# Kernel tuning notes

Measured on AMD Instinct MI355X. Metric: run time of the kernel, lower is better.

Reference implementation:

```python
import jax, jax.numpy as jnp
import numpy as np

WEIGHT = 1.0
EPS = 1e-10


def _high_mask(h, w):
    # Boolean mask: True = high-frequency region (outside center rectangle after fftshift)
    mask = np.ones((h, w), dtype=np.float32)
    ch, cw = h // 2, w // 2
    mask[ch - h // 8: ch + h // 8, cw - w // 8: cw + w // 8] = 0.0
    return jnp.asarray(mask)


def _high_freq_psd(img):
    # img: (B, 3, H, W) in [-1, 1] -> per-image mean log10 PSD over high-freq region, shape (B,)
    gray = 0.299 * img[:, 0] + 0.587 * img[:, 1] + 0.114 * img[:, 2]  # (B, H, W)
    gray = (gray + 1.0) / 2.0
    fft = jnp.fft.fft2(gray)                       # batched complex FFT over last two dims
    fft = jnp.fft.fftshift(fft, axes=(-2, -1))
    psd_log = jnp.log10(jnp.abs(fft) ** 2 + EPS)   # (B, H, W)
    h, w = gray.shape[-2:]
    mask = _high_mask(h, w)
    return jnp.sum(psd_log * mask, axis=(-2, -1)) / jnp.sum(mask)


def setup_inputs() -> dict:
    key = jax.random.key(0)
    k1, k2 = jax.random.split(key)
    B, C, H, W = 32, 3, 512, 512
    generated = jax.random.normal(k1, (B, C, H, W), dtype=jnp.float32)
    target = jax.random.normal(k2, (B, C, H, W), dtype=jnp.float32)
    return {"generated": generated, "target": target}


def reference(generated, target):
    psd_gen = _high_freq_psd(generated)      # (B,)
    psd_target = _high_freq_psd(target)      # (B,)
    loss = jnp.mean(jnp.abs(psd_gen - psd_target))  # F.l1_loss
    return WEIGHT * loss
```

## Files before the change

### kernel.cpp

```cpp
#include <hip/hip_runtime.h>
#include <hip/hip_bf16.h>
#include <hip/hip_fp16.h>
#include <math.h>


__device__ double g_partials[64 * 17 * 4];
__device__ __align__(16) __half2 g_ws[(size_t)64 * 256 * 512];

__device__ __forceinline__ float2 cadd(float2 a, float2 b){ return make_float2(a.x+b.x, a.y+b.y); }
__device__ __forceinline__ float2 csub(float2 a, float2 b){ return make_float2(a.x-b.x, a.y-b.y); }
__device__ __forceinline__ float2 cmul(float2 a, float2 b){
  return make_float2(fmaf(a.x, b.x, -(a.y*b.y)), fmaf(a.x, b.y, a.y*b.x));
}
__device__ __forceinline__ float2 mul_mi(float2 a){ return make_float2(a.y, -a.x); }

__device__ __forceinline__ void fft8(float2 v[8]){
  const float S = 0.70710678118654752440f;
  float2 c0=cadd(v[0],v[4]), c1=cadd(v[1],v[5]), c2=cadd(v[2],v[6]), c3=cadd(v[3],v[7]);
  float2 d0=csub(v[0],v[4]);
  float2 t1=csub(v[1],v[5]);
  float2 d1=make_float2(S*(t1.x+t1.y), S*(t1.y-t1.x));
  float2 d2=mul_mi(csub(v[2],v[6]));
  float2 t3=csub(v[3],v[7]);
  float2 d3=make_float2(S*(t3.y-t3.x), -S*(t3.x+t3.y));
  float2 e0=cadd(c0,c2), e1=cadd(c1,c3), f0=csub(c0,c2), f1=mul_mi(csub(c1,c3));
  float2 g0=cadd(d0,d2), g1=cadd(d1,d3), h0=csub(d0,d2), h1=mul_mi(csub(d1,d3));
  v[0]=cadd(e0,e1); v[4]=csub(e0,e1);
  v[2]=cadd(f0,f1); v[6]=csub(f0,f1);
  v[1]=cadd(g0,g1); v[5]=csub(g0,g1);
  v[3]=cadd(h0,h1); v[7]=csub(h0,h1);
}

__device__ __forceinline__ void twiddle8(float2 v[8], float ang){
  float sn, cs;
  __sincosf(ang, &sn, &cs);
  float2 w = make_float2(cs, sn);
  float2 wp = w;
  v[1] = cmul(v[1], wp);
  #pragma unroll
  for (int m = 2; m < 8; ++m){ wp = cmul(wp, w); v[m] = cmul(v[m], wp); }
}

__device__ __forceinline__ int padi(int i){ return i + (i >> 3); }

__device__ __forceinline__ void lds_fence(){
  asm volatile("s_waitcnt lgkmcnt(0)" ::: "memory");
  __builtin_amdgcn_sched_barrier(0);
}

__device__ __forceinline__ void fft512(float2 v[8], float* re, float* im, int t){
  const float TW = -6.28318530717958647692f;
  fft8(v);
  twiddle8(v, TW * (float)t * (1.0f/512.0f));
  lds_fence();
  #pragma unroll
  for (int m = 0; m < 8; ++m){ int a = padi(m*64 + t); re[a] = v[m].x; im[a] = v[m].y; }
  lds_fence();
  const int q = t >> 3, n = t & 7;
  #pragma unroll
  for (int j = 0; j < 8; ++j){ int a = padi(q*64 + n + 8*j); v[j].x = re[a]; v[j].y = im[a]; }
  fft8(v);
  twiddle8(v, TW * (float)n * (1.0f/64.0f));
  lds_fence();
  #pragma unroll
  for (int m = 0; m < 8; ++m){ int a = padi(q*64 + m*8 + n); re[a] = v[m].x; im[a] = v[m].y; }
  lds_fence();
  #pragma unroll
  for (int j = 0; j < 8; ++j){ int a = padi(q*64 + n*8 + j); v[j].x = re[a]; v[j].y = im[a]; }
  fft8(v);
}

#define GRAY1(r,g,b) ((fmaf(0.299f,(r), fmaf(0.587f,(g), 0.114f*(b))) + 1.0f)*0.5f)

__device__ __forceinline__ void dma_pair(const float* base, float* st, int t){
  #pragma unroll
  for (int ch = 0; ch < 3; ++ch){
    const float* pb = base + ch * 262144 + 4*t;
    float* lb = st + ch*1024;
    #pragma unroll
    for (int seg = 0; seg < 4; ++seg){
      __builtin_amdgcn_global_load_lds(
        (const __attribute__((address_space(1))) void*)(pb + seg*256),
        (__attribute__((address_space(3))) void*)(lb + seg*256),
        16, 0, 0);
    }
  }
}

__global__ __launch_bounds__(128)
void k_rowfft(const float* __restrict__ gen, const float* __restrict__ tgt){
  const int wg   = blockIdx.x;
  const int img  = wg >> 4;
  const int bl   = wg & 15;
  const int wave = threadIdx.x >> 6, t = threadIdx.x & 63;
  const int prB  = bl*16 + wave*8;
  const float* src = (img < 32) ? gen : tgt;
  const float* base0 = src + (size_t)(img & 31) * 786432 + (size_t)prB * 1024;

  __shared__ float stage_all[2][2][3072];
  float* stg0 = stage_all[wave][0];
  float* stg1 = stage_all[wave][1];

  const int off = 8*(t & 7) + (t >> 3);

  dma_pair(base0, stg0, t);
  #pragma unroll
  for (int n = 0; n < 8; ++n){
    float* stc = (n & 1) ? stg1 : stg0;
    float* stn = (n & 1) ? stg0 : stg1;
    lds_fence();
    if (n < 7) dma_pair(base0 + (size_t)(n+1)*1024, stn, t);
    if (n == 0)      { asm volatile("s_waitcnt vmcnt(12)" ::: "memory"); }
    else if (n < 7)  { asm volatile("s_waitcnt vmcnt(20)" ::: "memory"); }
    else             { asm volatile("s_waitcnt vmcnt(8)"  ::: "memory"); }
    __builtin_amdgcn_sched_barrier(0);

    float2 v[8];
    #pragma unroll
    for (int j = 0; j < 8; ++j){
      const int x = t + 64*j;
      v[j] = make_float2(GRAY1(stc[x],     stc[1024+x], stc[2048+x]),
                         GRAY1(stc[512+x], stc[1536+x], stc[2560+x]));
    }
    fft512(v, stc, stc + 1024, t);

    __half2* dst = g_ws + ((size_t)img * 256 + (prB + n)) * 512;
    #pragma unroll
    for (int j = 0; j < 8; ++j) dst[64*j + off] = __floats2half2_rn(v[j].x, v[j].y);
  }
}

__global__ __launch_bounds__(256)
void k_colfft(){
  const int wg   = blockIdx.x;
  const int img  = wg / 17;
  const int blk  = wg - img * 17;
  const int kx0  = blk * 16;
  const int tid  = threadIdx.x;
  const int wave = tid >> 6, t = tid & 63;
  const int ncols = (blk == 16) ? 1 : 16;

  __shared__ __half2 own[16 * 258], mir[16 * 258];
  __shared__ float re_all[4][576], im_all[4][576];
  float* re = re_all[wave];
  float* im = im_all[wave];

  const __half2* zb = g_ws + (size_t)img * 131072;
  #pragma unroll
  for (int it = 0; it < 16; ++it){
    const int idx = it*256 + tid;
    const int p = idx >> 4, e = idx & 15;
    own[e*258 + p] = zb[p*512 + kx0 + e];
    mir[e*258 + p] = zb[p*512 + ((512 - (kx0 + e)) & 511)];
  }
  __syncthreads();

  double acc = 0.0;
  for (int ci = 0; ci < 4; ++ci){
    const int e = wave*4 + ci;
    if (e < ncols){
      const int kx = kx0 + e;
      const bool sub_own = (kx <= 63);
      const bool sub_mir = (kx >= 1) & (kx <= 64);
      const float base = (kx == 0 || kx == 256) ? 1.0f : 2.0f;

      float2 v[8];
      const int u = t >> 1;
      const bool odd = (t & 1);
      #pragma unroll
      for (int j = 0; j < 8; ++j){
        const int p = u + 32*j;
        float2 A = __half22float2(own[e*258 + p]);
        float2 B = __half22float2(mir[e*258 + p]); B.y = -B.y;
        float2 Fe = make_float2((A.x + B.x)*0.5f, (A.y + B.y)*0.5f);
        float2 Fo = mul_mi(make_float2((A.x - B.x)*0.5f, (A.y - B.y)*0.5f));
        v[j] = odd ? Fo : Fe;
      }
      fft512(v, re, im, t);

      #pragma unroll
      for (int j = 0; j < 8; ++j){
        const bool inS  = (j == 0) | (j == 7);
        const bool inSp = (j == 0) | ((j == 1) & (t == 0)) | ((j == 7) & (t != 0));
        float wgt = base;
        if (sub_own & inS)  wgt -= 1.0f;
        if (sub_mir & inSp) wgt -= 1.0f;
        float m2 = fmaf(v[j].x, v[j].x, fmaf(v[j].y, v[j].y, 1e-10f));
        acc += (double)wgt * (double)log10f(m2);
      }
    }
  }
  #pragma unroll
  for (int off = 32; off; off >>= 1) acc += __shfl_down(acc, off);
  if (t == 0) g_partials[((size_t)img * 17 + blk) * 4 + wave] = acc;
}

__global__ __launch_bounds__(256)
void k_finish(float* __restrict__ out){
  const int tid = threadIdx.x;
  const int img = tid >> 2, part = tid & 3;
  const double* p = g_partials + (size_t)img * 68 + part;
  double s = 0.0;
  for (int k = 0; k < 17; ++k) s += p[4*k];
  __shared__ double sm[256];
  sm[tid] = s;
  __syncthreads();
  if ((tid & 3) == 0){
    double tot = sm[tid] + sm[tid+1] + sm[tid+2] + sm[tid+3];
    sm[tid] = tot * (1.0 / 245760.0);
  }
  __syncthreads();
  if (tid < 64){
    double dv = (tid < 32) ? fabs(sm[tid*4] - sm[(tid+32)*4]) : 0.0;
    #pragma unroll
    for (int off = 32; off; off >>= 1) dv += __shfl_down(dv, off);
    if (tid == 0) out[0] = (float)(dv * (1.0 / 32.0));
  }
}

extern "C" void kernel_launch(void* const* d_in, const int* in_sizes, int n_in,
                              void* d_out, int out_size, void* d_ws, size_t ws_size,
                              hipStream_t stream){
  (void)in_sizes; (void)n_in; (void)out_size; (void)d_ws; (void)ws_size;
  const float* gen = (const float*)d_in[0];
  const float* tgt = (const float*)d_in[1];
  float* out = (float*)d_out;

  k_rowfft<<<dim3(64 * 16), dim3(128), 0, stream>>>(gen, tgt);
  k_colfft<<<dim3(64 * 17), dim3(256), 0, stream>>>();
  k_finish<<<dim3(1), dim3(256), 0, stream>>>(out);
}
```

Before: 70.64 us.

## Replace LDS DMA staging with register double-buffered float4 loads in row FFT

The row FFT kernel no longer stages raw RGB rows into LDS through global_load_lds DMA. It loads float4 vectors into two register buffers, converts to gray in registers and writes only the gray values into a small padded LDS area per wave. Blocks grow from 2 to 4 waves and each wave handles 4 row pairs instead of 8. The aim is to cut LDS footprint and traffic and to raise occupancy and parallelism, at the cost of many more VGPRs for the register buffers (96 floats per thread).

```diff
diff --git a/kernel.cpp b/kernel.cpp
--- a/kernel.cpp
+++ b/kernel.cpp
@@ -72,59 +72,68 @@
 
 #define GRAY1(r,g,b) ((fmaf(0.299f,(r), fmaf(0.587f,(g), 0.114f*(b))) + 1.0f)*0.5f)
 
-__device__ __forceinline__ void dma_pair(const float* base, float* st, int t){
-  #pragma unroll
-  for (int ch = 0; ch < 3; ++ch){
-    const float* pb = base + ch * 262144 + 4*t;
-    float* lb = st + ch*1024;
-    #pragma unroll
-    for (int seg = 0; seg < 4; ++seg){
-      __builtin_amdgcn_global_load_lds(
-        (const __attribute__((address_space(1))) void*)(pb + seg*256),
-        (__attribute__((address_space(3))) void*)(lb + seg*256),
-        16, 0, 0);
-    }
-  }
-}
-
-__global__ __launch_bounds__(128)
+__global__ __launch_bounds__(256, 4)
 void k_rowfft(const float* __restrict__ gen, const float* __restrict__ tgt){
   const int wg   = blockIdx.x;
   const int img  = wg >> 4;
   const int bl   = wg & 15;
   const int wave = threadIdx.x >> 6, t = threadIdx.x & 63;
-  const int prB  = bl*16 + wave*8;
+  const int pr0  = bl*16 + wave*4;
   const float* src = (img < 32) ? gen : tgt;
-  const float* base0 = src + (size_t)(img & 31) * 786432 + (size_t)prB * 1024;
-
-  __shared__ float stage_all[2][2][3072];
-  float* stg0 = stage_all[wave][0];
-  float* stg1 = stage_all[wave][1];
+  const float4* f4 = (const float4*)(src + (size_t)(img & 31) * 786432
+                                         + (size_t)pr0 * 1024) + t;
+
+  __shared__ float ex_all[4][1184];
+  float* re = ex_all[wave];
+  float* im = ex_all[wave] + 576;
 
   const int off = 8*(t & 7) + (t >> 3);
 
-  dma_pair(base0, stg0, t);
-  #pragma unroll
-  for (int n = 0; n < 8; ++n){
-    float* stc = (n & 1) ? stg1 : stg0;
-    float* stn = (n & 1) ? stg0 : stg1;
+  float4 bufA[12], bufB[12];
+  #pragma unroll
+  for (int c = 0; c < 3; ++c)
+    #pragma unroll
+    for (int s = 0; s < 4; ++s) bufA[c*4+s] = f4[c*65536 + s*64];
+
+  #pragma unroll
+  for (int n = 0; n < 4; ++n){
+    const float4* cur = (n & 1) ? bufB : bufA;
+    float4*       nxt = (n & 1) ? bufA : bufB;
+
+    #pragma unroll
+    for (int s = 0; s < 2; ++s){
+      const int x = s*256 + 4*t;
+      float4 r = cur[0+s], g = cur[4+s], b = cur[8+s];
+      re[padi(x+0)] = GRAY1(r.x, g.x, b.x);
+      re[padi(x+1)] = GRAY1(r.y, g.y, b.y);
+      re[padi(x+2)] = GRAY1(r.z, g.z, b.z);
+      re[padi(x+3)] = GRAY1(r.w, g.w, b.w);
+      float4 r2 = cur[2+s], g2 = cur[6+s], b2 = cur[10+s];
+      im[padi(x+0)] = GRAY1(r2.x, g2.x, b2.x);
+      im[padi(x+1)] = GRAY1(r2.y, g2.y, b2.y);
+      im[padi(x+2)] = GRAY1(r2.z, g2.z, b2.z);
+      im[padi(x+3)] = GRAY1(r2.w, g2.w, b2.w);
+    }
+
+    if (n < 3){
+      #pragma unroll
+      for (int c = 0; c < 3; ++c)
+        #pragma unroll
+        for (int s = 0; s < 4; ++s)
+          nxt[c*4+s] = f4[(n+1)*256 + c*65536 + s*64];
+      __builtin_amdgcn_sched_barrier(0);
+    }
+
     lds_fence();
-    if (n < 7) dma_pair(base0 + (size_t)(n+1)*1024, stn, t);
-    if (n == 0)      { asm volatile("s_waitcnt vmcnt(12)" ::: "memory"); }
-    else if (n < 7)  { asm volatile("s_waitcnt vmcnt(20)" ::: "memory"); }
-    else             { asm volatile("s_waitcnt vmcnt(8)"  ::: "memory"); }
-    __builtin_amdgcn_sched_barrier(0);
-
     float2 v[8];
     #pragma unroll
     for (int j = 0; j < 8; ++j){
-      const int x = t + 64*j;
-      v[j] = make_float2(GRAY1(stc[x],     stc[1024+x], stc[2048+x]),
-                         GRAY1(stc[512+x], stc[1536+x], stc[2560+x]));
-    }
-    fft512(v, stc, stc + 1024, t);
-
-    __half2* dst = g_ws + ((size_t)img * 256 + (prB + n)) * 512;
+      const int a = padi(t + 64*j);
+      v[j] = make_float2(re[a], im[a]);
+    }
+    fft512(v, re, im, t);
+
+    __half2* dst = g_ws + ((size_t)img * 256 + (pr0 + n)) * 512;
     #pragma unroll
     for (int j = 0; j < 8; ++j) dst[64*j + off] = __floats2half2_rn(v[j].x, v[j].y);
   }
@@ -226,7 +235,7 @@
   const float* tgt = (const float*)d_in[1];
   float* out = (float*)d_out;
 
-  k_rowfft<<<dim3(64 * 16), dim3(128), 0, stream>>>(gen, tgt);
+  k_rowfft<<<dim3(64 * 16), dim3(256), 0, stream>>>(gen, tgt);
   k_colfft<<<dim3(64 * 17), dim3(256), 0, stream>>>();
   k_finish<<<dim3(1), dim3(256), 0, stream>>>(out);
 }
```

Result: slower. 76.43 us (+8.2%).

## Fold final reduction into column FFT via last-block ticket, ping-pong row FFT LDS

Applied to the files above, without the earlier changes.

Removes the separate k_finish launch. The last column-FFT block, found through an atomic ticket counter that the row kernel resets, now performs the final reduction. The row FFT's second LDS transpose writes to a separate staging region, which drops one LDS fence per FFT. This trades a kernel launch and a barrier for an atomic plus threadfences in every column block.

```diff
diff --git a/kernel.cpp b/kernel.cpp
--- a/kernel.cpp
+++ b/kernel.cpp
@@ -5,6 +5,7 @@
 
 
 __device__ double g_partials[64 * 17 * 4];
+__device__ int    g_done;
 __device__ __align__(16) __half2 g_ws[(size_t)64 * 256 * 512];
 
 __device__ __forceinline__ float2 cadd(float2 a, float2 b){ return make_float2(a.x+b.x, a.y+b.y); }
@@ -70,6 +71,28 @@
   fft8(v);
 }
 
+__device__ __forceinline__ void fft512pp(float2 v[8], float* re1, float* im1,
+                                         float* re2, float* im2, int t){
+  const float TW = -6.28318530717958647692f;
+  fft8(v);
+  twiddle8(v, TW * (float)t * (1.0f/512.0f));
+  lds_fence();
+  #pragma unroll
+  for (int m = 0; m < 8; ++m){ int a = padi(m*64 + t); re1[a] = v[m].x; im1[a] = v[m].y; }
+  lds_fence();
+  const int q = t >> 3, n = t & 7;
+  #pragma unroll
+  for (int j = 0; j < 8; ++j){ int a = padi(q*64 + n + 8*j); v[j].x = re1[a]; v[j].y = im1[a]; }
+  fft8(v);
+  twiddle8(v, TW * (float)n * (1.0f/64.0f));
+  #pragma unroll
+  for (int m = 0; m < 8; ++m){ int a = padi(q*64 + m*8 + n); re2[a] = v[m].x; im2[a] = v[m].y; }
+  lds_fence();
+  #pragma unroll
+  for (int j = 0; j < 8; ++j){ int a = padi(q*64 + n*8 + j); v[j].x = re2[a]; v[j].y = im2[a]; }
+  fft8(v);
+}
+
 #define GRAY1(r,g,b) ((fmaf(0.299f,(r), fmaf(0.587f,(g), 0.114f*(b))) + 1.0f)*0.5f)
 
 __device__ __forceinline__ void dma_pair(const float* base, float* st, int t){
@@ -89,6 +112,7 @@
 
 __global__ __launch_bounds__(128)
 void k_rowfft(const float* __restrict__ gen, const float* __restrict__ tgt){
+  if (blockIdx.x == 0 && threadIdx.x == 0) g_done = 0;
   const int wg   = blockIdx.x;
   const int img  = wg >> 4;
   const int bl   = wg & 15;
@@ -122,7 +146,7 @@
       v[j] = make_float2(GRAY1(stc[x],     stc[1024+x], stc[2048+x]),
                          GRAY1(stc[512+x], stc[1536+x], stc[2560+x]));
     }
-    fft512(v, stc, stc + 1024, t);
+    fft512pp(v, stc, stc + 1024, stc + 1600, stc + 2176, t);
 
     __half2* dst = g_ws + ((size_t)img * 256 + (prB + n)) * 512;
     #pragma unroll
@@ -131,7 +155,7 @@
 }
 
 __global__ __launch_bounds__(256)
-void k_colfft(){
+void k_colfft(float* __restrict__ out){
   const int wg   = blockIdx.x;
   const int img  = wg / 17;
   const int blk  = wg - img * 17;
@@ -142,6 +166,7 @@
 
   __shared__ __half2 own[16 * 258], mir[16 * 258];
   __shared__ float re_all[4][576], im_all[4][576];
+  __shared__ int ticket;
   float* re = re_all[wave];
   float* im = im_all[wave];
 
@@ -193,28 +218,31 @@
   #pragma unroll
   for (int off = 32; off; off >>= 1) acc += __shfl_down(acc, off);
   if (t == 0) g_partials[((size_t)img * 17 + blk) * 4 + wave] = acc;
-}
-
-__global__ __launch_bounds__(256)
-void k_finish(float* __restrict__ out){
-  const int tid = threadIdx.x;
-  const int img = tid >> 2, part = tid & 3;
-  const double* p = g_partials + (size_t)img * 68 + part;
-  double s = 0.0;
-  for (int k = 0; k < 17; ++k) s += p[4*k];
-  __shared__ double sm[256];
-  sm[tid] = s;
+
   __syncthreads();
-  if ((tid & 3) == 0){
-    double tot = sm[tid] + sm[tid+1] + sm[tid+2] + sm[tid+3];
-    sm[tid] = tot * (1.0 / 245760.0);
-  }
+  __threadfence();
+  if (tid == 0) ticket = atomicAdd(&g_done, 1);
   __syncthreads();
-  if (tid < 64){
-    double dv = (tid < 32) ? fabs(sm[tid*4] - sm[(tid+32)*4]) : 0.0;
-    #pragma unroll
-    for (int off = 32; off; off >>= 1) dv += __shfl_down(dv, off);
-    if (tid == 0) out[0] = (float)(dv * (1.0 / 32.0));
+  if (ticket == 64*17 - 1){
+    __threadfence();
+    const int fim = tid >> 2, part = tid & 3;
+    const double* p = g_partials + (size_t)fim * 68 + part;
+    double s = 0.0;
+    for (int k = 0; k < 17; ++k) s += p[4*k];
+    __shared__ double sm[256];
+    sm[tid] = s;
+    __syncthreads();
+    if ((tid & 3) == 0){
+      double tot = sm[tid] + sm[tid+1] + sm[tid+2] + sm[tid+3];
+      sm[tid] = tot * (1.0 / 245760.0);
+    }
+    __syncthreads();
+    if (tid < 64){
+      double dv = (tid < 32) ? fabs(sm[tid*4] - sm[(tid+32)*4]) : 0.0;
+      #pragma unroll
+      for (int off = 32; off; off >>= 1) dv += __shfl_down(dv, off);
+      if (tid == 0) out[0] = (float)(dv * (1.0 / 32.0));
+    }
   }
 }
 
@@ -227,6 +255,5 @@
   float* out = (float*)d_out;
 
   k_rowfft<<<dim3(64 * 16), dim3(128), 0, stream>>>(gen, tgt);
-  k_colfft<<<dim3(64 * 17), dim3(256), 0, stream>>>();
-  k_finish<<<dim3(1), dim3(256), 0, stream>>>(out);
-}
+  k_colfft<<<dim3(64 * 17), dim3(256), 0, stream>>>(out);
+}
```

Measured after the change: 133.1 us. 88.4% more time.

## Replace LDS-transposed FFT512 stages with cross-lane shuffle butterflies

Applied to the files above, without the earlier changes.

Reworks the 512-point FFT so the two inner radix-8 stages use __shfl_xor butterflies across the 64 lanes, with per-lane precomputed twiddles, instead of round trips through LDS with fences. The row kernel now writes bit-reversed output as two 16-byte vector stores per lane, and the column kernel drops its per-wave LDS scratch. The mask weighting and the vmcnt waits are adjusted to match the new output ordering. This removes LDS traffic and waits but adds many shuffle instructions (6 stages × 8 × 2) and more registers for twiddles.

```diff
diff --git a/kernel.cpp b/kernel.cpp
--- a/kernel.cpp
+++ b/kernel.cpp
@@ -13,6 +13,7 @@
   return make_float2(fmaf(a.x, b.x, -(a.y*b.y)), fmaf(a.x, b.y, a.y*b.x));
 }
 __device__ __forceinline__ float2 mul_mi(float2 a){ return make_float2(a.y, -a.x); }
+__device__ __forceinline__ int br3(int x){ return ((x&1)<<2) | (x&2) | ((x>>2)&1); }
 
 __device__ __forceinline__ void fft8(float2 v[8]){
   const float S = 0.70710678118654752440f;
@@ -31,43 +32,76 @@
   v[3]=cadd(h0,h1); v[7]=csub(h0,h1);
 }
 
-__device__ __forceinline__ void twiddle8(float2 v[8], float ang){
+__device__ __forceinline__ float2 shflx(float2 x, int m){
+  return make_float2(__shfl_xor(x.x, m, 64), __shfl_xor(x.y, m, 64));
+}
+
+__device__ __forceinline__ void bfly(float2 v[8], int maskbit, bool hi, float2 w){
+  #pragma unroll
+  for (int m = 0; m < 8; ++m){
+    float2 u = shflx(v[m], maskbit);
+    float2 s = cmul(csub(u, v[m]), w);
+    float2 a = cadd(v[m], u);
+    v[m] = hi ? s : a;
+  }
+}
+__device__ __forceinline__ void bfly_nw(float2 v[8], int maskbit, bool hi){
+  #pragma unroll
+  for (int m = 0; m < 8; ++m){
+    float2 u = shflx(v[m], maskbit);
+    float2 s = csub(u, v[m]);
+    float2 a = cadd(v[m], u);
+    v[m] = hi ? s : a;
+  }
+}
+
+struct LaneTw {
+  float2 wp[7];
+  float2 wA1, wA2, wB1, wB2;
+  float2 w25;
+};
+
+__device__ __forceinline__ LaneTw make_lanetw(int t){
+  LaneTw L;
+  const float TW = -6.28318530717958647692f;
+  const float S  = 0.70710678118654752440f;
   float sn, cs;
-  __sincosf(ang, &sn, &cs);
-  float2 w = make_float2(cs, sn);
-  float2 wp = w;
-  v[1] = cmul(v[1], wp);
-  #pragma unroll
-  for (int m = 2; m < 8; ++m){ wp = cmul(wp, w); v[m] = cmul(v[m], wp); }
-}
-
-__device__ __forceinline__ int padi(int i){ return i + (i >> 3); }
+  __sincosf(TW * (float)t * (1.0f/512.0f), &sn, &cs);
+  float2 w1 = make_float2(cs, sn);
+  L.wp[0] = w1;
+  #pragma unroll
+  for (int i = 1; i < 7; ++i) L.wp[i] = cmul(L.wp[i-1], w1);
+  const int a = t >> 3, b = t & 7;
+  const int ea = a & 3, eb = b & 3;
+  L.wA1 = make_float2((ea==0)?1.0f:(ea==1)?S:(ea==2)?0.0f:-S,
+                      (ea==0)?0.0f:(ea==1)?-S:(ea==2)?-1.0f:-S);
+  L.wB1 = make_float2((eb==0)?1.0f:(eb==1)?S:(eb==2)?0.0f:-S,
+                      (eb==0)?0.0f:(eb==1)?-S:(eb==2)?-1.0f:-S);
+  L.wA2 = (a & 1) ? make_float2(0.0f,-1.0f) : make_float2(1.0f,0.0f);
+  L.wB2 = (b & 1) ? make_float2(0.0f,-1.0f) : make_float2(1.0f,0.0f);
+  const int k1 = br3(a);
+  __sincosf(TW * (float)(b * k1) * (1.0f/64.0f), &sn, &cs);
+  L.w25 = make_float2(cs, sn);
+  return L;
+}
+
+__device__ __forceinline__ void fft512x(float2 v[8], const LaneTw& L, int t){
+  fft8(v);
+  #pragma unroll
+  for (int m = 1; m < 8; ++m) v[m] = cmul(v[m], L.wp[m-1]);
+  bfly   (v, 32, (t & 32) != 0, L.wA1);
+  bfly   (v, 16, (t & 16) != 0, L.wA2);
+  bfly_nw(v, 8,  (t & 8)  != 0);
+  #pragma unroll
+  for (int m = 0; m < 8; ++m) v[m] = cmul(v[m], L.w25);
+  bfly   (v, 4, (t & 4) != 0, L.wB1);
+  bfly   (v, 2, (t & 2) != 0, L.wB2);
+  bfly_nw(v, 1, (t & 1) != 0);
+}
 
 __device__ __forceinline__ void lds_fence(){
   asm volatile("s_waitcnt lgkmcnt(0)" ::: "memory");
   __builtin_amdgcn_sched_barrier(0);
-}
-
-__device__ __forceinline__ void fft512(float2 v[8], float* re, float* im, int t){
-  const float TW = -6.28318530717958647692f;
-  fft8(v);
-  twiddle8(v, TW * (float)t * (1.0f/512.0f));
-  lds_fence();
-  #pragma unroll
-  for (int m = 0; m < 8; ++m){ int a = padi(m*64 + t); re[a] = v[m].x; im[a] = v[m].y; }
-  lds_fence();
-  const int q = t >> 3, n = t & 7;
-  #pragma unroll
-  for (int j = 0; j < 8; ++j){ int a = padi(q*64 + n + 8*j); v[j].x = re[a]; v[j].y = im[a]; }
-  fft8(v);
-  twiddle8(v, TW * (float)n * (1.0f/64.0f));
-  lds_fence();
-  #pragma unroll
-  for (int m = 0; m < 8; ++m){ int a = padi(q*64 + m*8 + n); re[a] = v[m].x; im[a] = v[m].y; }
-  lds_fence();
-  #pragma unroll
-  for (int j = 0; j < 8; ++j){ int a = padi(q*64 + n*8 + j); v[j].x = re[a]; v[j].y = im[a]; }
-  fft8(v);
 }
 
 #define GRAY1(r,g,b) ((fmaf(0.299f,(r), fmaf(0.587f,(g), 0.114f*(b))) + 1.0f)*0.5f)
@@ -101,7 +135,8 @@
   float* stg0 = stage_all[wave][0];
   float* stg1 = stage_all[wave][1];
 
-  const int off = 8*(t & 7) + (t >> 3);
+  const LaneTw L = make_lanetw(t);
+  const int kbase = 8*br3(t >> 3) + 64*br3(t & 7);
 
   dma_pair(base0, stg0, t);
   #pragma unroll
@@ -111,8 +146,8 @@
     lds_fence();
     if (n < 7) dma_pair(base0 + (size_t)(n+1)*1024, stn, t);
     if (n == 0)      { asm volatile("s_waitcnt vmcnt(12)" ::: "memory"); }
-    else if (n < 7)  { asm volatile("s_waitcnt vmcnt(20)" ::: "memory"); }
-    else             { asm volatile("s_waitcnt vmcnt(8)"  ::: "memory"); }
+    else if (n < 7)  { asm volatile("s_waitcnt vmcnt(14)" ::: "memory"); }
+    else             { asm volatile("s_waitcnt vmcnt(2)"  ::: "memory"); }
     __builtin_amdgcn_sched_barrier(0);
 
     float2 v[8];
@@ -122,11 +157,15 @@
       v[j] = make_float2(GRAY1(stc[x],     stc[1024+x], stc[2048+x]),
                          GRAY1(stc[512+x], stc[1536+x], stc[2560+x]));
     }
-    fft512(v, stc, stc + 1024, t);
-
-    __half2* dst = g_ws + ((size_t)img * 256 + (prB + n)) * 512;
-    #pragma unroll
-    for (int j = 0; j < 8; ++j) dst[64*j + off] = __floats2half2_rn(v[j].x, v[j].y);
+    fft512x(v, L, t);
+
+    __half2 h[8];
+    #pragma unroll
+    for (int m = 0; m < 8; ++m) h[m] = __floats2half2_rn(v[m].x, v[m].y);
+    uint4* dst = (uint4*)(g_ws + ((size_t)img * 256 + (prB + n)) * 512 + kbase);
+    const uint4* hp = (const uint4*)h;
+    dst[0] = hp[0];
+    dst[1] = hp[1];
   }
 }
 
@@ -141,9 +180,6 @@
   const int ncols = (blk == 16) ? 1 : 16;
 
   __shared__ __half2 own[16 * 258], mir[16 * 258];
-  __shared__ float re_all[4][576], im_all[4][576];
-  float* re = re_all[wave];
-  float* im = im_all[wave];
 
   const __half2* zb = g_ws + (size_t)img * 131072;
   #pragma unroll
@@ -154,6 +190,10 @@
     mir[e*258 + p] = zb[p*512 + ((512 - (kx0 + e)) & 511)];
   }
   __syncthreads();
+
+  const LaneTw L = make_lanetw(t);
+  const int pa = t >> 3, pb = t & 7;
+  const bool inS = (pb == 0) | (pb == 7);
 
   double acc = 0.0;
   for (int ci = 0; ci < 4; ++ci){
@@ -162,7 +202,7 @@
       const int kx = kx0 + e;
       const bool sub_own = (kx <= 63);
       const bool sub_mir = (kx >= 1) & (kx <= 64);
-      const float base = (kx == 0 || kx == 256) ? 1.0f : 2.0f;
+      const float wbase = (kx == 0 || kx == 256) ? 1.0f : 2.0f;
 
       float2 v[8];
       const int u = t >> 1;
@@ -176,16 +216,17 @@
         float2 Fo = mul_mi(make_float2((A.x - B.x)*0.5f, (A.y - B.y)*0.5f));
         v[j] = odd ? Fo : Fe;
       }
-      fft512(v, re, im, t);
+      fft512x(v, L, t);
 
       #pragma unroll
-      for (int j = 0; j < 8; ++j){
-        const bool inS  = (j == 0) | (j == 7);
-        const bool inSp = (j == 0) | ((j == 1) & (t == 0)) | ((j == 7) & (t != 0));
-        float wgt = base;
+      for (int m = 0; m < 8; ++m){
+        const bool m0 = (m == 0);
+        const bool inSp = (pb == 0) | ((pb == 4) & (pa == 0) & m0)
+                        | ((pb == 7) & !((pa == 0) & m0));
+        float wgt = wbase;
         if (sub_own & inS)  wgt -= 1.0f;
         if (sub_mir & inSp) wgt -= 1.0f;
-        float m2 = fmaf(v[j].x, v[j].x, fmaf(v[j].y, v[j].y, 1e-10f));
+        float m2 = fmaf(v[m].x, v[m].x, fmaf(v[m].y, v[m].y, 1e-10f));
         acc += (double)wgt * (double)log10f(m2);
       }
     }
```

New measurement: 99.01 us. +40.2%, slower.
